# Performance work log

Hardware: AMD Instinct MI355X
Metric: run time of the kernel (lower is better)

Reference implementation:

```python
import jax, jax.numpy as jnp
import numpy as np

B, C, H, W = 4, 256, 64, 64
R = 8          # rank = min(8, C//4)
G = 4          # conv groups
CG = C // G    # channels per group


def conv1x1(x, w, b):
    # x: [B,C,H,W], w: [O,C], b: [O]
    return jnp.einsum('oc,bchw->bohw', w, x) + b[None, :, None, None]


def conv1x1_grouped(x, w, b):
    # x: [B,C,H,W], w: [C, C//G] (per-output-channel slice of its group), b: [C]
    xg = x.reshape(B, G, CG, H, W)
    wg = w.reshape(G, CG, CG)  # [group, out_in_group, in_in_group]
    out = jnp.einsum('goc,bgchw->bgohw', wg, xg).reshape(B, C, H, W)
    return out + b[None, :, None, None]


def attend(q, k, v):
    # q,k: [B,R,H,W]; v: [B,C,H,W]; N = H*W
    qf = q.reshape(B, R, H * W)
    kf = k.reshape(B, R, H * W)
    vf = v.reshape(B, C, H * W)
    scores = jnp.einsum('bri,brj->bij', qf, kf)       # [B,N,N], no 1/sqrt scaling (faithful)
    attn = jax.nn.softmax(scores, axis=-1)
    out = jnp.einsum('bcm,bmn->bcn', vf, attn)        # v @ attn, contraction over query index m
    return out.reshape(B, C, H, W)


def setup_inputs():
    key = jax.random.key(0)
    ks = jax.random.split(key, 10)
    s = 0.05
    return {
        'fL': jax.random.normal(ks[0], (B, C, H, W), jnp.float32),
        'fU': jax.random.normal(ks[1], (B, C, H, W), jnp.float32),
        'qL_w': jax.random.normal(ks[2], (R, C), jnp.float32) * s,
        'qL_b': jnp.zeros((R,), jnp.float32),
        'kU_w': jax.random.normal(ks[3], (R, C), jnp.float32) * s,
        'kU_b': jnp.zeros((R,), jnp.float32),
        'vU_w': jax.random.normal(ks[4], (C, CG), jnp.float32) * s,
        'vU_b': jnp.zeros((C,), jnp.float32),
        'qU_w': jax.random.normal(ks[5], (R, C), jnp.float32) * s,
        'qU_b': jnp.zeros((R,), jnp.float32),
        'kL_w': jax.random.normal(ks[6], (R, C), jnp.float32) * s,
        'kL_b': jnp.zeros((R,), jnp.float32),
        'vL_w': jax.random.normal(ks[7], (C, CG), jnp.float32) * s,
        'vL_b': jnp.zeros((C,), jnp.float32),
        'beta': jnp.array(0.5, jnp.float32),
    }


def reference(fL, fU, qL_w, qL_b, kU_w, kU_b, vU_w, vU_b,
              qU_w, qU_b, kL_w, kL_b, vL_w, vL_b, beta):
    LU = attend(conv1x1(fL, qL_w, qL_b),
                conv1x1(fU, kU_w, kU_b),
                conv1x1_grouped(fU, vU_w, vU_b))
    UL = attend(conv1x1(fU, qU_w, qU_b),
                conv1x1(fL, kL_w, kL_b),
                conv1x1_grouped(fL, vL_w, vL_b))
    fL2 = fL + beta * LU
    fU2 = fU + beta * UL
    return (fL2, fU2)
```

## Files before the change

kernel.cpp:

```cpp
#include <hip/hip_runtime.h>

typedef float f32x4 __attribute__((ext_vector_type(4)));
typedef float f32x16 __attribute__((ext_vector_type(16)));
typedef short s16x8 __attribute__((ext_vector_type(8)));
typedef unsigned short u16;
typedef unsigned long long u64;

#define BN 4
#define CC 256
#define NN 4096

static __device__ __forceinline__ u16 f2bf(float x) {
    unsigned int u = __float_as_uint(x);
    u += 0x7FFF + ((u >> 16) & 1);
    return (u16)(u >> 16);
}

__global__ __launch_bounds__(256) void k_wtrans(
    const float* __restrict__ qLw, const float* __restrict__ kLw,
    const float* __restrict__ qUw, const float* __restrict__ kUw,
    const float* __restrict__ vUw, const float* __restrict__ vLw,
    float* __restrict__ wT, float* __restrict__ wvT)
{
    int a = blockIdx.x, t = threadIdx.x;
    const float* qw = a ? qUw : qLw;
    const float* kw = a ? kUw : kLw;
#pragma unroll
    for (int r = 0; r < 8; ++r) {
        wT[((size_t)a * 256 + t) * 16 + r]     = qw[r * 256 + t];
        wT[((size_t)a * 256 + t) * 16 + 8 + r] = kw[r * 256 + t];
    }
    const float* wv = a ? vLw : vUw;
    for (int cp = 0; cp < 64; ++cp)
        wvT[((size_t)a * 64 + cp) * 256 + t] = wv[(size_t)t * 64 + cp];
}

__global__ __launch_bounds__(512) void k_qkprep(
    const float* __restrict__ fL, const float* __restrict__ fU,
    const float* __restrict__ wT,
    const float* __restrict__ qLb, const float* __restrict__ kLb,
    const float* __restrict__ qUb, const float* __restrict__ kUb,
    u16* __restrict__ qbf, u16* __restrict__ kbf)
{
    int blk = blockIdx.x;
    int nc = blk & 31, b = (blk >> 5) & 3, src = blk >> 7;
    const float* f = src ? fU : fL;
    int qa = src, ka = 1 - src;
    int t = threadIdx.x;
    int nl = t & 127;
    int cs = __builtin_amdgcn_readfirstlane(t >> 7) * 64;
    int n = nc * 128 + nl;
    const float* fp = f + (size_t)b * 256 * NN + n;
    const float* wbase = wT + (size_t)src * 4096;

    float acc[16];
#pragma unroll
    for (int r = 0; r < 16; ++r) acc[r] = 0.f;

#pragma unroll 4
    for (int c = cs; c < cs + 64; ++c) {
        float fv = fp[(size_t)c * NN];
        const float* wr = wbase + (size_t)c * 16;
#pragma unroll
        for (int r = 0; r < 16; ++r) acc[r] += wr[r] * fv;
    }

    __shared__ float red[4][128][17];
    int cc = t >> 7;
#pragma unroll
    for (int r = 0; r < 16; ++r) red[cc][nl][r] = acc[r];
    __syncthreads();

    if (t < 128) {
        const float* bq = src ? qUb : qLb;
        const float* bk = src ? kUb : kLb;
        const float L2E = 1.4426950408889634f;
        int nn = nc * 128 + t;
        u16 pq[8], pk[8];
#pragma unroll
        for (int r = 0; r < 8; ++r) {
            float sq = red[0][t][r] + red[1][t][r] + red[2][t][r] + red[3][t][r];
            float sk = red[0][t][8+r] + red[1][t][8+r] + red[2][t][8+r] + red[3][t][8+r];
            pq[r] = f2bf((sq + bq[r]) * L2E);
            pk[r] = f2bf( sk + bk[r]);
        }
        uint4 vq, vk;
        vq.x = pq[0] | ((unsigned)pq[1] << 16); vq.y = pq[2] | ((unsigned)pq[3] << 16);
        vq.z = pq[4] | ((unsigned)pq[5] << 16); vq.w = pq[6] | ((unsigned)pq[7] << 16);
        vk.x = pk[0] | ((unsigned)pk[1] << 16); vk.y = pk[2] | ((unsigned)pk[3] << 16);
        vk.z = pk[4] | ((unsigned)pk[5] << 16); vk.w = pk[6] | ((unsigned)pk[7] << 16);
        *(uint4*)(qbf + (((size_t)qa * BN + b) * NN + nn) * 8) = vq;
        *(uint4*)(kbf + (((size_t)ka * BN + b) * NN + nn) * 8) = vk;
    }
}

__global__ __launch_bounds__(256) void k_zsum(
    const u16* __restrict__ qbf, const u16* __restrict__ kbf,
    float* __restrict__ Z)
{
    int blk = blockIdx.x;
    int mt = blk & 31, ab = blk >> 5;
    int t = threadIdx.x, l = t & 63;
    int w = __builtin_amdgcn_readfirstlane(t >> 6);
    int l31 = l & 31, g2 = l >> 5;
    int m0 = mt * 128 + w * 32;

    const u16* qab = qbf + (size_t)ab * NN * 8;
    const u16* kab = kbf + (size_t)ab * NN * 8;

    s16x8 af = *(const s16x8*)(qab + (size_t)(m0 + l31) * 8);
    if (g2) af = (s16x8)0;

    auto ldb = [&](int i) -> s16x8 {
        s16x8 r = *(const s16x8*)(kab + (size_t)(i * 32 + l31) * 8);
        return g2 ? (s16x8)0 : r;
    };

    float zp[16];
#pragma unroll
    for (int r = 0; r < 16; ++r) zp[r] = 0.f;

    s16x8 b0 = ldb(0), b1 = ldb(1);
#pragma unroll 1
    for (int i = 0; i < 128; ++i) {
        int nx = i + 2 < 127 ? i + 2 : 127;
        s16x8 bn = ldb(nx);
        f32x16 s = __builtin_amdgcn_mfma_f32_32x32x16_bf16(af, b0, (f32x16)0.f, 0, 0, 0);
#pragma unroll
        for (int r = 0; r < 16; ++r) zp[r] += __builtin_exp2f(s[r]);
        b0 = b1; b1 = bn;
    }

#pragma unroll
    for (int r = 0; r < 16; ++r) {
        float v = zp[r];
#pragma unroll
        for (int d = 1; d < 32; d <<= 1) v += __shfl_xor(v, d, 64);
        zp[r] = v;
    }
    if (l31 == 0) {
#pragma unroll
        for (int r = 0; r < 16; ++r) {
            int m = m0 + (r & 3) + 8 * (r >> 2) + 4 * g2;
            Z[(size_t)ab * NN + m] = zp[r];
        }
    }
}

__global__ __launch_bounds__(256) void k_vprep(
    const float* __restrict__ fL, const float* __restrict__ fU,
    const float* __restrict__ wvT,
    const float* __restrict__ vUb, const float* __restrict__ vLb,
    const float* __restrict__ Z, u16* __restrict__ vpt)
{
    int blk = blockIdx.x;
    int mc = blk & 31, g = (blk >> 5) & 3, ab = blk >> 7;
    int a = ab >> 2, b = ab & 3;
    const float* f    = a ? fL : fU;
    const float* bias = a ? vLb : vUb;
    int t = threadIdx.x, l = t & 63;
    int wu = __builtin_amdgcn_readfirstlane(t >> 6);
    int m0 = mc * 128 + l * 2;

    const float* fg = f + ((size_t)b * 256 + g * 64) * NN + m0;
    const float* wq = wvT + (size_t)a * 16384 + g * 64 + wu * 16;

    float acc[16][2];
#pragma unroll
    for (int j = 0; j < 16; ++j) { acc[j][0] = 0.f; acc[j][1] = 0.f; }

    for (int cp = 0; cp < 64; ++cp) {
        float2 fv = *(const float2*)(fg + (size_t)cp * NN);
        const float* wr = wq + (size_t)cp * 256;
        float4 w0 = *(const float4*)(wr);
        float4 w1 = *(const float4*)(wr + 4);
        float4 w2 = *(const float4*)(wr + 8);
        float4 w3 = *(const float4*)(wr + 12);
        float wv[16] = {w0.x,w0.y,w0.z,w0.w, w1.x,w1.y,w1.z,w1.w,
                        w2.x,w2.y,w2.z,w2.w, w3.x,w3.y,w3.z,w3.w};
#pragma unroll
        for (int j = 0; j < 16; ++j) {
            acc[j][0] += wv[j] * fv.x;
            acc[j][1] += wv[j] * fv.y;
        }
    }

    float2 z = *(const float2*)(Z + (size_t)ab * NN + m0);
    float zr0 = 1.f / z.x, zr1 = 1.f / z.y;
    int mt = m0 >> 5, mi = m0 & 31;
    u16* vpo = vpt + (((size_t)ab * 128 + mt) * 256 + g * 64 + wu * 16) * 32 + mi;
#pragma unroll
    for (int j = 0; j < 16; ++j) {
        float bj = bias[g * 64 + wu * 16 + j];
        unsigned pk = (unsigned)f2bf((acc[j][0] + bj) * zr0) |
                      ((unsigned)f2bf((acc[j][1] + bj) * zr1) << 16);
        *(unsigned*)(vpo + (size_t)j * 32) = pk;
    }
}

__global__ __launch_bounds__(256, 4) void k_main(
    const float* __restrict__ fL, const float* __restrict__ fU,
    const u16* __restrict__ qbf, const u16* __restrict__ kbf,
    const u16* __restrict__ vpt, const float* __restrict__ beta_p,
    float* __restrict__ out)
{
    int blk = blockIdx.x;
    int ab = blk & 7, nt = (blk >> 3) & 63, cs = blk >> 9;
    int a = ab >> 2, b = ab & 3;
    int n0 = nt * 64;
    int t = threadIdx.x, l = t & 63;
    int w = __builtin_amdgcn_readfirstlane(t >> 6);
    int c15 = l & 15, g = l >> 4;

    __shared__ u16 ebuf[2][64][64];

    auto eptr = [&](int p, int n, int mbyte) -> char* {
        return ((char*)ebuf) + (((p << 6) + n) << 7) + (mbyte ^ ((n & 7) << 4));
    };

    const u16* qab = qbf + (size_t)ab * NN * 8;
    const u16* kab = kbf + (size_t)ab * NN * 8;

    s16x8 bkf = *(const s16x8*)(kab + (size_t)(n0 + w * 16 + c15) * 8);
    if (g) bkf = (s16x8)0;

    const u16* apb = vpt + (size_t)ab * (128ull * 8192)
                   + (size_t)(cs * 128 + w * 32 + c15) * 32 + g * 8;

    f32x4 acc[2][4];
#pragma unroll
    for (int i = 0; i < 2; ++i)
#pragma unroll
        for (int j = 0; j < 4; ++j) acc[i][j] = (f32x4)0.f;

    auto qld = [&](int win, int mq) -> s16x8 {
        s16x8 r = *(const s16x8*)(qab + (size_t)(win * 64 + mq * 16 + c15) * 8);
        return g ? (s16x8)0 : r;
    };

    auto egen = [&](int pbuf, const s16x8 (&qv)[4]) {
#pragma unroll
        for (int mq = 0; mq < 4; ++mq) {
            f32x4 s = __builtin_amdgcn_mfma_f32_16x16x32_bf16(qv[mq], bkf, (f32x4)0.f, 0, 0, 0);
            u64 pk = 0;
#pragma unroll
            for (int r = 0; r < 4; ++r)
                pk |= (u64)f2bf(__builtin_exp2f(s[r])) << (16 * r);
            *(u64*)eptr(pbuf, w * 16 + c15, mq * 32 + g * 8) = pk;
        }
    };

    {
        s16x8 q0[4];
#pragma unroll
        for (int mq = 0; mq < 4; ++mq) q0[mq] = qld(0, mq);
        egen(0, q0);
    }
    s16x8 qn[4];
#pragma unroll
    for (int mq = 0; mq < 4; ++mq) qn[mq] = qld(1, mq);

    s16x8 afc[2][2], afn[2][2];
#pragma unroll
    for (int cf = 0; cf < 2; ++cf) {
        afc[cf][0] = *(const s16x8*)(apb + cf * 512);
        afc[cf][1] = *(const s16x8*)(apb + 8192 + cf * 512);
    }
    __syncthreads();

#pragma unroll 1
    for (int k = 0; k < 64; ++k) {
        int p = k & 1;

        if (k < 63) {
            const u16* apn = apb + (size_t)(2 * (k + 1)) * 8192;
#pragma unroll
            for (int cf = 0; cf < 2; ++cf) {
                afn[cf][0] = *(const s16x8*)(apn + cf * 512);
                afn[cf][1] = *(const s16x8*)(apn + 8192 + cf * 512);
            }
            egen(p ^ 1, qn);
            if (k < 62) {
#pragma unroll
                for (int mq = 0; mq < 4; ++mq) qn[mq] = qld(k + 2, mq);
            }
        }

#pragma unroll
        for (int kc = 0; kc < 2; ++kc) {
            s16x8 bf[4];
#pragma unroll
            for (int nf = 0; nf < 4; ++nf)
                bf[nf] = *(const s16x8*)eptr(p, nf * 16 + c15, kc * 64 + g * 16);
#pragma unroll
            for (int cf = 0; cf < 2; ++cf)
#pragma unroll
                for (int nf = 0; nf < 4; ++nf)
                    acc[cf][nf] = __builtin_amdgcn_mfma_f32_16x16x32_bf16(
                        afc[cf][kc], bf[nf], acc[cf][nf], 0, 0, 0);
        }

#pragma unroll
        for (int cf = 0; cf < 2; ++cf) {
            afc[cf][0] = afn[cf][0];
            afc[cf][1] = afn[cf][1];
        }
        __syncthreads();
    }

    float beta = beta_p[0];
    const float* base = a ? fU : fL;
    float* op = out + (size_t)a * ((size_t)BN * CC * NN);
#pragma unroll
    for (int cf = 0; cf < 2; ++cf)
#pragma unroll
        for (int nf = 0; nf < 4; ++nf)
#pragma unroll
            for (int r = 0; r < 4; ++r) {
                int c = cs * 128 + w * 32 + cf * 16 + g * 4 + r;
                int n = n0 + nf * 16 + c15;
                size_t idx = ((size_t)b * CC + c) * NN + n;
                op[idx] = base[idx] + beta * acc[cf][nf][r];
            }
}

extern "C" void kernel_launch(void* const* d_in, const int* in_sizes, int n_in,
                              void* d_out, int out_size, void* d_ws, size_t ws_size,
                              hipStream_t stream) {
    const float* fL  = (const float*)d_in[0];
    const float* fU  = (const float*)d_in[1];
    const float* qLw = (const float*)d_in[2];
    const float* qLb = (const float*)d_in[3];
    const float* kUw = (const float*)d_in[4];
    const float* kUb = (const float*)d_in[5];
    const float* vUw = (const float*)d_in[6];
    const float* vUb = (const float*)d_in[7];
    const float* qUw = (const float*)d_in[8];
    const float* qUb = (const float*)d_in[9];
    const float* kLw = (const float*)d_in[10];
    const float* kLb = (const float*)d_in[11];
    const float* vLw = (const float*)d_in[12];
    const float* vLb = (const float*)d_in[13];
    const float* beta = (const float*)d_in[14];

    char* ws = (char*)d_ws;
    float* wT  = (float*)(ws);
    float* wvT = (float*)(ws + 32768);
    u16*   qbf = (u16*)  (ws + 163840);
    u16*   kbf = (u16*)  (ws + 688128);
    float* Z   = (float*)(ws + 1212416);
    u16*   vpt = (u16*)  (ws + 1343488);
    float* out = (float*)d_out;

    k_wtrans<<<2, 256, 0, stream>>>(qLw, kLw, qUw, kUw, vUw, vLw, wT, wvT);
    k_qkprep<<<256, 512, 0, stream>>>(fL, fU, wT, qLb, kLb, qUb, kUb, qbf, kbf);
    k_zsum<<<256, 256, 0, stream>>>(qbf, kbf, Z);
    k_vprep<<<1024, 256, 0, stream>>>(fL, fU, wvT, vUb, vLb, Z, vpt);
    k_main<<<1024, 256, 0, stream>>>(fL, fU, qbf, kbf, vpt, beta, out);
}
```

Before: 211.6 us.

## Enlarge main kernel tile to all channels and 128 keys, unroll pipeline

Each block of k_main now covers all 256 output channels and 128 key positions with 512 threads, so the exp(QK) tile is generated once per key window instead of once per channel half. This removes the duplicated score and exp computation across the two channel splits. The main loop is unrolled by two with a fixed buffer parity, and exp generation is interleaved between the LDS reads and the MFMAs. BF16 packing now uses the v_cvt_pk_bf16_f32 instruction. In exchange, accumulator registers double, the grid shrinks to 256 blocks, and occupancy drops.

```diff
diff --git a/kernel.cpp b/kernel.cpp
--- a/kernel.cpp
+++ b/kernel.cpp
@@ -198,24 +198,25 @@
     }
 }
 
-__global__ __launch_bounds__(256, 4) void k_main(
+__global__ __launch_bounds__(512) void k_main(
     const float* __restrict__ fL, const float* __restrict__ fU,
     const u16* __restrict__ qbf, const u16* __restrict__ kbf,
     const u16* __restrict__ vpt, const float* __restrict__ beta_p,
     float* __restrict__ out)
 {
     int blk = blockIdx.x;
-    int ab = blk & 7, nt = (blk >> 3) & 63, cs = blk >> 9;
+    int ab = blk & 7, nt = blk >> 3;
     int a = ab >> 2, b = ab & 3;
-    int n0 = nt * 64;
+    int n0 = nt * 128;
     int t = threadIdx.x, l = t & 63;
     int w = __builtin_amdgcn_readfirstlane(t >> 6);
     int c15 = l & 15, g = l >> 4;
-
-    __shared__ u16 ebuf[2][64][64];
+    int swz = (c15 & 7) << 4;
+
+    __shared__ u16 ebuf[2][128][64];
 
     auto eptr = [&](int p, int n, int mbyte) -> char* {
-        return ((char*)ebuf) + (((p << 6) + n) << 7) + (mbyte ^ ((n & 7) << 4));
+        return ((char*)ebuf) + (((p << 7) + n) << 7) + (mbyte ^ swz);
     };
 
     const u16* qab = qbf + (size_t)ab * NN * 8;
@@ -225,13 +226,13 @@
     if (g) bkf = (s16x8)0;
 
     const u16* apb = vpt + (size_t)ab * (128ull * 8192)
-                   + (size_t)(cs * 128 + w * 32 + c15) * 32 + g * 8;
-
-    f32x4 acc[2][4];
+                   + (size_t)(w * 32 + c15) * 32 + g * 8;
+
+    f32x4 acc[2][8];
 #pragma unroll
     for (int i = 0; i < 2; ++i)
 #pragma unroll
-        for (int j = 0; j < 4; ++j) acc[i][j] = (f32x4)0.f;
+        for (int j = 0; j < 8; ++j) acc[i][j] = (f32x4)0.f;
 
     auto qld = [&](int win, int mq) -> s16x8 {
         s16x8 r = *(const s16x8*)(qab + (size_t)(win * 64 + mq * 16 + c15) * 8);
@@ -242,12 +243,56 @@
 #pragma unroll
         for (int mq = 0; mq < 4; ++mq) {
             f32x4 s = __builtin_amdgcn_mfma_f32_16x16x32_bf16(qv[mq], bkf, (f32x4)0.f, 0, 0, 0);
-            u64 pk = 0;
-#pragma unroll
-            for (int r = 0; r < 4; ++r)
-                pk |= (u64)f2bf(__builtin_exp2f(s[r])) << (16 * r);
-            *(u64*)eptr(pbuf, w * 16 + c15, mq * 32 + g * 8) = pk;
-        }
+            float e0 = __builtin_exp2f(s[0]);
+            float e1 = __builtin_exp2f(s[1]);
+            float e2 = __builtin_exp2f(s[2]);
+            float e3 = __builtin_exp2f(s[3]);
+            unsigned lo, hi;
+            asm("v_cvt_pk_bf16_f32 %0, %1, %2" : "=v"(lo) : "v"(e0), "v"(e1));
+            asm("v_cvt_pk_bf16_f32 %0, %1, %2" : "=v"(hi) : "v"(e2), "v"(e3));
+            uint2 pk; pk.x = lo; pk.y = hi;
+            *(uint2*)eptr(pbuf, w * 16 + c15, mq * 32 + g * 8) = pk;
+        }
+    };
+
+    s16x8 qn[4];
+    s16x8 afc[2][2], afn[2][2];
+
+    auto step = [&](int P, int kn, int kq, bool do_egen) {
+        const u16* apn = apb + (size_t)(2 * kn) * 8192;
+#pragma unroll
+        for (int cf = 0; cf < 2; ++cf) {
+            afn[cf][0] = *(const s16x8*)(apn + cf * 512);
+            afn[cf][1] = *(const s16x8*)(apn + 8192 + cf * 512);
+        }
+        s16x8 bf[8];
+#pragma unroll
+        for (int nf = 0; nf < 8; ++nf)
+            bf[nf] = *(const s16x8*)eptr(P, nf * 16 + c15, g * 16);
+        if (do_egen) egen(P ^ 1, qn);
+#pragma unroll
+        for (int cf = 0; cf < 2; ++cf)
+#pragma unroll
+            for (int nf = 0; nf < 8; ++nf)
+                acc[cf][nf] = __builtin_amdgcn_mfma_f32_16x16x32_bf16(
+                    afc[cf][0], bf[nf], acc[cf][nf], 0, 0, 0);
+#pragma unroll
+        for (int nf = 0; nf < 8; ++nf)
+            bf[nf] = *(const s16x8*)eptr(P, nf * 16 + c15, 64 + g * 16);
+#pragma unroll
+        for (int cf = 0; cf < 2; ++cf)
+#pragma unroll
+            for (int nf = 0; nf < 8; ++nf)
+                acc[cf][nf] = __builtin_amdgcn_mfma_f32_16x16x32_bf16(
+                    afc[cf][1], bf[nf], acc[cf][nf], 0, 0, 0);
+#pragma unroll
+        for (int mq = 0; mq < 4; ++mq) qn[mq] = qld(kq, mq);
+#pragma unroll
+        for (int cf = 0; cf < 2; ++cf) {
+            afc[cf][0] = afn[cf][0];
+            afc[cf][1] = afn[cf][1];
+        }
+        __syncthreads();
     };
 
     {
@@ -256,11 +301,8 @@
         for (int mq = 0; mq < 4; ++mq) q0[mq] = qld(0, mq);
         egen(0, q0);
     }
-    s16x8 qn[4];
 #pragma unroll
     for (int mq = 0; mq < 4; ++mq) qn[mq] = qld(1, mq);
-
-    s16x8 afc[2][2], afn[2][2];
 #pragma unroll
     for (int cf = 0; cf < 2; ++cf) {
         afc[cf][0] = *(const s16x8*)(apb + cf * 512);
@@ -269,43 +311,12 @@
     __syncthreads();
 
 #pragma unroll 1
-    for (int k = 0; k < 64; ++k) {
-        int p = k & 1;
-
-        if (k < 63) {
-            const u16* apn = apb + (size_t)(2 * (k + 1)) * 8192;
-#pragma unroll
-            for (int cf = 0; cf < 2; ++cf) {
-                afn[cf][0] = *(const s16x8*)(apn + cf * 512);
-                afn[cf][1] = *(const s16x8*)(apn + 8192 + cf * 512);
-            }
-            egen(p ^ 1, qn);
-            if (k < 62) {
-#pragma unroll
-                for (int mq = 0; mq < 4; ++mq) qn[mq] = qld(k + 2, mq);
-            }
-        }
-
-#pragma unroll
-        for (int kc = 0; kc < 2; ++kc) {
-            s16x8 bf[4];
-#pragma unroll
-            for (int nf = 0; nf < 4; ++nf)
-                bf[nf] = *(const s16x8*)eptr(p, nf * 16 + c15, kc * 64 + g * 16);
-#pragma unroll
-            for (int cf = 0; cf < 2; ++cf)
-#pragma unroll
-                for (int nf = 0; nf < 4; ++nf)
-                    acc[cf][nf] = __builtin_amdgcn_mfma_f32_16x16x32_bf16(
-                        afc[cf][kc], bf[nf], acc[cf][nf], 0, 0, 0);
-        }
-
-#pragma unroll
-        for (int cf = 0; cf < 2; ++cf) {
-            afc[cf][0] = afn[cf][0];
-            afc[cf][1] = afn[cf][1];
-        }
-        __syncthreads();
+    for (int k2 = 0; k2 < 32; ++k2) {
+        int ke = 2 * k2;
+        step(0, ke + 1, ke + 2 < 63 ? ke + 2 : 63, true);
+        int ko = 2 * k2 + 1;
+        int kn = ko + 1 < 63 ? ko + 1 : 63;
+        step(1, kn, ko + 2 < 63 ? ko + 2 : 63, k2 < 31);
     }
 
     float beta = beta_p[0];
@@ -314,10 +325,10 @@
 #pragma unroll
     for (int cf = 0; cf < 2; ++cf)
 #pragma unroll
-        for (int nf = 0; nf < 4; ++nf)
+        for (int nf = 0; nf < 8; ++nf)
 #pragma unroll
             for (int r = 0; r < 4; ++r) {
-                int c = cs * 128 + w * 32 + cf * 16 + g * 4 + r;
+                int c = w * 32 + cf * 16 + g * 4 + r;
                 int n = n0 + nf * 16 + c15;
                 size_t idx = ((size_t)b * CC + c) * NN + n;
                 op[idx] = base[idx] + beta * acc[cf][nf][r];
@@ -356,5 +367,5 @@
     k_qkprep<<<256, 512, 0, stream>>>(fL, fU, wT, qLb, kLb, qUb, kUb, qbf, kbf);
     k_zsum<<<256, 256, 0, stream>>>(qbf, kbf, Z);
     k_vprep<<<1024, 256, 0, stream>>>(fL, fU, wvT, vUb, vLb, Z, vpt);
-    k_main<<<1024, 256, 0, stream>>>(fL, fU, qbf, kbf, vpt, beta, out);
-}
+    k_main<<<256, 512, 0, stream>>>(fL, fU, qbf, kbf, vpt, beta, out);
+}
```

Measured after the change: 180.3 us. 14.8% less time.
